# Kernel tuning notes

Hardware: AMD Instinct MI355X
Metric: run time of the kernel (lower is better)

The kernel has to match this reference:

```python
import jax, jax.numpy as jnp
import numpy as np

E, T, IN, OUT = 8, 16384, 1024, 1024  # n_groups, total_tokens, in_features, out_features


def setup_inputs() -> dict:
    key = jax.random.key(0)
    kx, kw, ks = jax.random.split(key, 3)
    x = jax.random.normal(kx, (T, IN), dtype=jnp.float32)
    # kaiming_uniform-ish scale for weight [E, OUT, IN]
    weight = jax.random.normal(kw, (E, OUT, IN), dtype=jnp.float32) * (1.0 / np.sqrt(IN))
    # ragged segment lengths that sum exactly to T (random cut points)
    cuts = jnp.sort(jax.random.randint(ks, (E - 1,), 0, T + 1)).astype(jnp.int32)
    seg_lens = jnp.diff(
        jnp.concatenate([jnp.zeros((1,), jnp.int32), cuts, jnp.full((1,), T, jnp.int32)])
    )
    return {"x": x, "weight": weight, "seg_lens": seg_lens}


def reference(x, weight, seg_lens):
    # Grouped GEMM: row t of x is multiplied by weight[g(t)].T where g(t) is the
    # segment (expert) that token t falls into per seg_lens. trans_b=True.
    n_groups = weight.shape[0]
    bounds = jnp.cumsum(seg_lens)                                  # [E]
    seg_id = jnp.searchsorted(bounds, jnp.arange(x.shape[0]), side="right")  # [T]
    y = jnp.zeros((x.shape[0], weight.shape[1]), dtype=x.dtype)
    for e in range(n_groups):  # small fixed loop over groups
        y = y + jnp.where((seg_id == e)[:, None], x @ weight[e].T, 0)
    return y
```

## Files before the change

### kernel.cpp

```cpp
#include <hip/hip_runtime.h>

#define T_TOK  16384
#define IN_F   1024
#define OUT_F  1024
#define NE     8
#define BM     128
#define BN     128
#define BK     32
#define NTHREADS 256
#define ROW_TILE_SLOTS 136

typedef __bf16 bf16;
typedef bf16  bf16x4 __attribute__((ext_vector_type(4)));
typedef bf16  bf16x8 __attribute__((ext_vector_type(8)));
typedef float f32x4  __attribute__((ext_vector_type(4)));

__global__ __launch_bounds__(NTHREADS)
void grouped_gemm_f32io_bf16(const float* __restrict__ x,
                             const float* __restrict__ wgt,
                             const int*  __restrict__ seg_lens,
                             float* __restrict__ out)
{
    __shared__ __align__(16) bf16 As[BM * BK];
    __shared__ __align__(16) bf16 Bs[BN * BK];

    const int m    = blockIdx.y;
    const int col0 = blockIdx.x * BN;

    int e_sel = -1, row0 = 0, rows = 0;
    {
        int start = 0, acct = 0;
        #pragma unroll
        for (int e = 0; e < NE; ++e) {
            int len = seg_lens[e];
            int nt  = (len + BM - 1) >> 7;
            if (e_sel < 0 && m >= acct && m < acct + nt) {
                e_sel = e;
                row0  = start + (m - acct) * BM;
                int rem = start + len - row0;
                rows = rem < BM ? rem : BM;
            }
            acct  += nt;
            start += len;
        }
    }
    if (e_sel < 0) return;

    const int tid  = threadIdx.x;
    const int lane = tid & 63;
    const int wave = tid >> 6;
    const int wm   = (wave >> 1) * 64;
    const int wn   = (wave & 1) * 64;
    const int quad = lane >> 4;
    const int l16  = lane & 15;

    const float* wbase = wgt + ((size_t)e_sel * OUT_F + (size_t)col0) * IN_F;

    f32x4 acc[4][4] = {};

    for (int k0 = 0; k0 < IN_F; k0 += BK) {
        f32x4 a_st[4], b_st[4];
        #pragma unroll
        for (int t = 0; t < 4; ++t) {
            int c  = t * NTHREADS + tid;
            int rg = row0 + (c >> 3);
            if (rg > T_TOK - 1) rg = T_TOK - 1;
            a_st[t] = *(const f32x4*)(x + (size_t)rg * IN_F + k0 + (c & 7) * 4);
            b_st[t] = *(const f32x4*)(wbase + (size_t)(c >> 3) * IN_F + k0 + (c & 7) * 4);
        }

        __syncthreads();

        #pragma unroll
        for (int t = 0; t < 4; ++t) {
            int c = t * NTHREADS + tid;
            bf16x4 ha, hb;
            #pragma unroll
            for (int j = 0; j < 4; ++j) { ha[j] = (bf16)a_st[t][j]; hb[j] = (bf16)b_st[t][j]; }
            *(bf16x4*)(&As[(c >> 3) * BK + (c & 7) * 4]) = ha;
            *(bf16x4*)(&Bs[(c >> 3) * BK + (c & 7) * 4]) = hb;
        }
        __syncthreads();

        bf16x8 af[4], bfr[4];
        #pragma unroll
        for (int t = 0; t < 4; ++t)
            af[t] = *(const bf16x8*)(&As[(wm + t * 16 + l16) * BK + quad * 8]);
        #pragma unroll
        for (int u = 0; u < 4; ++u)
            bfr[u] = *(const bf16x8*)(&Bs[(wn + u * 16 + l16) * BK + quad * 8]);

        #pragma unroll
        for (int t = 0; t < 4; ++t)
            #pragma unroll
            for (int u = 0; u < 4; ++u)
                acc[t][u] = __builtin_amdgcn_mfma_f32_16x16x32_bf16(
                    af[t], bfr[u], acc[t][u], 0, 0, 0);
    }

    #pragma unroll
    for (int t = 0; t < 4; ++t) {
        #pragma unroll
        for (int r = 0; r < 4; ++r) {
            int row = wm + t * 16 + quad * 4 + r;
            if (row < rows) {
                size_t ob = (size_t)(row0 + row) * OUT_F + col0;
                #pragma unroll
                for (int u = 0; u < 4; ++u)
                    out[ob + wn + u * 16 + l16] = acc[t][u][r];
            }
        }
    }
}

extern "C" void kernel_launch(void* const* d_in, const int* in_sizes, int n_in,
                              void* d_out, int out_size, void* d_ws, size_t ws_size,
                              hipStream_t stream) {
    const float* x   = (const float*)d_in[0];
    const float* wgt = (const float*)d_in[1];
    const int*   seg = (const int*)d_in[2];
    float* out = (float*)d_out;

    dim3 grid(OUT_F / BN, ROW_TILE_SLOTS, 1);
    dim3 block(NTHREADS, 1, 1);
    grouped_gemm_f32io_bf16<<<grid, block, 0, stream>>>(x, wgt, seg, out);
}
```

Baseline: 216.0 us.

## Double-buffer shared memory tiles and prefetch next K-slice during MFMA

Splits the LDS A/B tiles into two buffers and issues global loads for the next K-slice before the MFMA work on the current slice. The bf16 conversion and LDS store into the alternate buffer happen after the MFMAs, so one barrier per iteration replaces two. This is meant to hide global load latency behind compute. In exchange it doubles LDS use to 32 KB per block and keeps the prefetched registers live across the MFMA loop.

```diff
diff --git a/kernel.cpp b/kernel.cpp
--- a/kernel.cpp
+++ b/kernel.cpp
@@ -21,8 +21,8 @@
                              const int*  __restrict__ seg_lens,
                              float* __restrict__ out)
 {
-    __shared__ __align__(16) bf16 As[BM * BK];
-    __shared__ __align__(16) bf16 Bs[BN * BK];
+    __shared__ __align__(16) bf16 As[2][BM * BK];
+    __shared__ __align__(16) bf16 Bs[2][BN * BK];
 
     const int m    = blockIdx.y;
     const int col0 = blockIdx.x * BN;
@@ -56,39 +56,58 @@
 
     const float* wbase = wgt + ((size_t)e_sel * OUT_F + (size_t)col0) * IN_F;
 
+    const float* ap[4];
+    const float* bp[4];
+    int lofs[4];
+    #pragma unroll
+    for (int t = 0; t < 4; ++t) {
+        int c  = t * NTHREADS + tid;
+        int rg = row0 + (c >> 3);
+        if (rg > T_TOK - 1) rg = T_TOK - 1;
+        ap[t]   = x + (size_t)rg * IN_F + (c & 7) * 4;
+        bp[t]   = wbase + (size_t)(c >> 3) * IN_F + (c & 7) * 4;
+        lofs[t] = (c >> 3) * BK + (c & 7) * 4;
+    }
+
+    f32x4 a_st[4], b_st[4];
+
+    #pragma unroll
+    for (int t = 0; t < 4; ++t) {
+        a_st[t] = *(const f32x4*)(ap[t]);
+        b_st[t] = *(const f32x4*)(bp[t]);
+    }
+    #pragma unroll
+    for (int t = 0; t < 4; ++t) {
+        bf16x4 ha, hb;
+        #pragma unroll
+        for (int j = 0; j < 4; ++j) { ha[j] = (bf16)a_st[t][j]; hb[j] = (bf16)b_st[t][j]; }
+        *(bf16x4*)(&As[0][lofs[t]]) = ha;
+        *(bf16x4*)(&Bs[0][lofs[t]]) = hb;
+    }
+    __syncthreads();
+
     f32x4 acc[4][4] = {};
+    int cur = 0;
 
     for (int k0 = 0; k0 < IN_F; k0 += BK) {
-        f32x4 a_st[4], b_st[4];
-        #pragma unroll
-        for (int t = 0; t < 4; ++t) {
-            int c  = t * NTHREADS + tid;
-            int rg = row0 + (c >> 3);
-            if (rg > T_TOK - 1) rg = T_TOK - 1;
-            a_st[t] = *(const f32x4*)(x + (size_t)rg * IN_F + k0 + (c & 7) * 4);
-            b_st[t] = *(const f32x4*)(wbase + (size_t)(c >> 3) * IN_F + k0 + (c & 7) * 4);
+        const int  kn = k0 + BK;
+        const bool pf = (kn < IN_F);
+
+        if (pf) {
+            #pragma unroll
+            for (int t = 0; t < 4; ++t) {
+                a_st[t] = *(const f32x4*)(ap[t] + kn);
+                b_st[t] = *(const f32x4*)(bp[t] + kn);
+            }
         }
-
-        __syncthreads();
-
-        #pragma unroll
-        for (int t = 0; t < 4; ++t) {
-            int c = t * NTHREADS + tid;
-            bf16x4 ha, hb;
-            #pragma unroll
-            for (int j = 0; j < 4; ++j) { ha[j] = (bf16)a_st[t][j]; hb[j] = (bf16)b_st[t][j]; }
-            *(bf16x4*)(&As[(c >> 3) * BK + (c & 7) * 4]) = ha;
-            *(bf16x4*)(&Bs[(c >> 3) * BK + (c & 7) * 4]) = hb;
-        }
-        __syncthreads();
 
         bf16x8 af[4], bfr[4];
         #pragma unroll
         for (int t = 0; t < 4; ++t)
-            af[t] = *(const bf16x8*)(&As[(wm + t * 16 + l16) * BK + quad * 8]);
+            af[t] = *(const bf16x8*)(&As[cur][(wm + t * 16 + l16) * BK + quad * 8]);
         #pragma unroll
         for (int u = 0; u < 4; ++u)
-            bfr[u] = *(const bf16x8*)(&Bs[(wn + u * 16 + l16) * BK + quad * 8]);
+            bfr[u] = *(const bf16x8*)(&Bs[cur][(wn + u * 16 + l16) * BK + quad * 8]);
 
         #pragma unroll
         for (int t = 0; t < 4; ++t)
@@ -96,6 +115,19 @@
             for (int u = 0; u < 4; ++u)
                 acc[t][u] = __builtin_amdgcn_mfma_f32_16x16x32_bf16(
                     af[t], bfr[u], acc[t][u], 0, 0, 0);
+
+        if (pf) {
+            #pragma unroll
+            for (int t = 0; t < 4; ++t) {
+                bf16x4 ha, hb;
+                #pragma unroll
+                for (int j = 0; j < 4; ++j) { ha[j] = (bf16)a_st[t][j]; hb[j] = (bf16)b_st[t][j]; }
+                *(bf16x4*)(&As[cur ^ 1][lofs[t]]) = ha;
+                *(bf16x4*)(&Bs[cur ^ 1][lofs[t]]) = hb;
+            }
+        }
+        __syncthreads();
+        cur ^= 1;
     }
 
     #pragma unroll
```

Result: slower. 227.1 us (+5.1%).

## Pre-convert inputs to bf16 in workspace and load tiles directly into LDS

Applied to the files above, without the earlier changes.

Adds a conversion kernel that casts x and all expert weights from fp32 to bf16 in the workspace. The GEMM kernel then reads the bf16 copies with global_load_lds, which writes 16-byte chunks straight into shared memory with no register staging or per-tile conversion. This halves operand bytes per tile and avoids the weight tiles being re-converted by every row-tile block. The cost is an extra pass over x and W (read fp32, write bf16) and a second launch. A fallback to the old kernel remains when the workspace is too small.

```diff
diff --git a/kernel.cpp b/kernel.cpp
--- a/kernel.cpp
+++ b/kernel.cpp
@@ -15,6 +15,130 @@
 typedef bf16  bf16x8 __attribute__((ext_vector_type(8)));
 typedef float f32x4  __attribute__((ext_vector_type(4)));
 
+#define NX_CHUNKS (T_TOK * IN_F / 4)
+#define NW_CHUNKS (NE * OUT_F * IN_F / 4)
+#define NTOT_CHUNKS (NX_CHUNKS + NW_CHUNKS)
+
+__global__ __launch_bounds__(NTHREADS)
+void cvt_f32_to_bf16(const float* __restrict__ x, const float* __restrict__ w,
+                     bf16* __restrict__ xb, bf16* __restrict__ wb)
+{
+    for (int i = blockIdx.x * NTHREADS + threadIdx.x; i < NTOT_CHUNKS;
+         i += gridDim.x * NTHREADS) {
+        const bool isx = (i < NX_CHUNKS);
+        const int  j   = isx ? i : i - NX_CHUNKS;
+        f32x4 v = isx ? ((const f32x4*)x)[j] : ((const f32x4*)w)[j];
+        bf16x4 h;
+        #pragma unroll
+        for (int k = 0; k < 4; ++k) h[k] = (bf16)v[k];
+        if (isx) ((bf16x4*)xb)[j] = h;
+        else     ((bf16x4*)wb)[j] = h;
+    }
+}
+
+__device__ __forceinline__ void gld_lds16(const bf16* g, bf16* l) {
+    __builtin_amdgcn_global_load_lds(
+        (const __attribute__((address_space(1))) void*)g,
+        (__attribute__((address_space(3))) void*)l,
+        16, 0, 0);
+}
+
+__global__ __launch_bounds__(NTHREADS)
+void grouped_gemm_bf16(const bf16* __restrict__ xb,
+                       const bf16* __restrict__ wb,
+                       const int*  __restrict__ seg_lens,
+                       float* __restrict__ out)
+{
+    __shared__ __align__(16) bf16 As[BM * BK];
+    __shared__ __align__(16) bf16 Bs[BN * BK];
+
+    const int m    = blockIdx.y;
+    const int col0 = blockIdx.x * BN;
+
+    int e_sel = -1, row0 = 0, rows = 0;
+    {
+        int start = 0, acct = 0;
+        #pragma unroll
+        for (int e = 0; e < NE; ++e) {
+            int len = seg_lens[e];
+            int nt  = (len + BM - 1) >> 7;
+            if (e_sel < 0 && m >= acct && m < acct + nt) {
+                e_sel = e;
+                row0  = start + (m - acct) * BM;
+                int rem = start + len - row0;
+                rows = rem < BM ? rem : BM;
+            }
+            acct  += nt;
+            start += len;
+        }
+    }
+    if (e_sel < 0) return;
+
+    const int tid  = threadIdx.x;
+    const int lane = tid & 63;
+    const int wave = tid >> 6;
+    const int wm   = (wave >> 1) * 64;
+    const int wn   = (wave & 1) * 64;
+    const int quad = lane >> 4;
+    const int l16  = lane & 15;
+
+    const bf16* wbase = wb + ((size_t)e_sel * OUT_F + (size_t)col0) * IN_F;
+
+    const int grp0 = wave * 16 + (lane >> 2);
+    const int kofs = (lane & 3) * 8;
+    int rgA0 = row0 + grp0;          if (rgA0 > T_TOK - 1) rgA0 = T_TOK - 1;
+    int rgA1 = row0 + grp0 + 64;     if (rgA1 > T_TOK - 1) rgA1 = T_TOK - 1;
+    const bf16* gA0 = xb + (size_t)rgA0 * IN_F + kofs;
+    const bf16* gA1 = xb + (size_t)rgA1 * IN_F + kofs;
+    const bf16* gB0 = wbase + (size_t)grp0 * IN_F + kofs;
+    const bf16* gB1 = wbase + (size_t)(grp0 + 64) * IN_F + kofs;
+    bf16* lA0 = As + wave * 512;
+    bf16* lA1 = As + (4 + wave) * 512;
+    bf16* lB0 = Bs + wave * 512;
+    bf16* lB1 = Bs + (4 + wave) * 512;
+
+    f32x4 acc[4][4] = {};
+
+    for (int k0 = 0; k0 < IN_F; k0 += BK) {
+        gld_lds16(gA0 + k0, lA0);
+        gld_lds16(gA1 + k0, lA1);
+        gld_lds16(gB0 + k0, lB0);
+        gld_lds16(gB1 + k0, lB1);
+        __syncthreads();
+
+        bf16x8 af[4], bfr[4];
+        #pragma unroll
+        for (int t = 0; t < 4; ++t)
+            af[t] = *(const bf16x8*)(&As[(wm + t * 16 + l16) * BK + quad * 8]);
+        #pragma unroll
+        for (int u = 0; u < 4; ++u)
+            bfr[u] = *(const bf16x8*)(&Bs[(wn + u * 16 + l16) * BK + quad * 8]);
+
+        #pragma unroll
+        for (int t = 0; t < 4; ++t)
+            #pragma unroll
+            for (int u = 0; u < 4; ++u)
+                acc[t][u] = __builtin_amdgcn_mfma_f32_16x16x32_bf16(
+                    af[t], bfr[u], acc[t][u], 0, 0, 0);
+
+        __syncthreads();
+    }
+
+    #pragma unroll
+    for (int t = 0; t < 4; ++t) {
+        #pragma unroll
+        for (int r = 0; r < 4; ++r) {
+            int row = wm + t * 16 + quad * 4 + r;
+            if (row < rows) {
+                size_t ob = (size_t)(row0 + row) * OUT_F + col0;
+                #pragma unroll
+                for (int u = 0; u < 4; ++u)
+                    out[ob + wn + u * 16 + l16] = acc[t][u][r];
+            }
+        }
+    }
+}
+
 __global__ __launch_bounds__(NTHREADS)
 void grouped_gemm_f32io_bf16(const float* __restrict__ x,
                              const float* __restrict__ wgt,
@@ -121,7 +245,18 @@
     const int*   seg = (const int*)d_in[2];
     float* out = (float*)d_out;
 
+    const size_t xbytes = (size_t)T_TOK * IN_F * sizeof(bf16);
+    const size_t wbytes = (size_t)NE * OUT_F * IN_F * sizeof(bf16);
+
     dim3 grid(OUT_F / BN, ROW_TILE_SLOTS, 1);
     dim3 block(NTHREADS, 1, 1);
-    grouped_gemm_f32io_bf16<<<grid, block, 0, stream>>>(x, wgt, seg, out);
-}
+
+    if (ws_size >= xbytes + wbytes) {
+        bf16* xb = (bf16*)d_ws;
+        bf16* wb = (bf16*)((char*)d_ws + xbytes);
+        cvt_f32_to_bf16<<<dim3(2048, 1, 1), block, 0, stream>>>(x, wgt, xb, wb);
+        grouped_gemm_bf16<<<grid, block, 0, stream>>>(xb, wb, seg, out);
+    } else {
+        grouped_gemm_f32io_bf16<<<grid, block, 0, stream>>>(x, wgt, seg, out);
+    }
+}
```

Result: no change. 218.7 us (+1.2%).
